# Performance work log

Measured on AMD Instinct MI355X. Metric: run time of the kernel, lower is better.

## Reference

```python
import jax, jax.numpy as jnp
import numpy as np

N, E, H, C, HC = 16384, 262144, 4, 128, 512
G, IN, ED, OUT, NCLS = 8, 5, 2, 256, 12
EPS = 1e-5


def _gatv2(x, src, dst, ea, Wl, Wr, We, att, b):
    # GATv2Conv (PyG): score = att . leaky_relu(lin_l(x_j) + lin_r(x_i) + lin_e(e))
    xl = (x @ Wl).reshape(-1, H, C)          # source transform [N,H,C]
    xr = (x @ Wr).reshape(-1, H, C)          # target transform [N,H,C]
    ee = (ea @ We).reshape(-1, H, C)         # edge embedding   [E,H,C]
    s = jax.nn.leaky_relu(xl[src] + xr[dst] + ee, 0.2)
    logit = jnp.einsum('ehc,hc->eh', s, att)            # [E,H]
    m = jax.ops.segment_max(logit, dst, num_segments=N)  # per-dst max
    a = jnp.exp(logit - m[dst])
    denom = jax.ops.segment_sum(a, dst, num_segments=N)
    alpha = a / (denom[dst] + 1e-16)                     # segment softmax
    out = jax.ops.segment_sum(xl[src] * alpha[:, :, None], dst, num_segments=N)
    return out.reshape(-1, HC) + b


def _bn(x, g, b):  # BatchNorm1d, training-mode batch stats
    mu = x.mean(0)
    var = x.var(0)
    return g * (x - mu) * jax.lax.rsqrt(var + EPS) + b


def setup_inputs() -> dict:
    key = jax.random.key(0)
    ks = iter(jax.random.split(key, 32))
    d = {}
    d['x'] = jax.random.normal(next(ks), (N, IN), jnp.float32)
    d['edge_attr'] = jax.random.normal(next(ks), (E, ED), jnp.float32)
    d['edge_index'] = jax.random.randint(next(ks), (2, E), 0, N)
    d['batch'] = jnp.sort(jax.random.randint(next(ks), (N,), 0, G))
    for i, din in zip((1, 2, 3), (IN, HC, HC)):
        d[f'c{i}_Wl'] = jax.random.normal(next(ks), (din, HC), jnp.float32) * 0.05
        d[f'c{i}_Wr'] = jax.random.normal(next(ks), (din, HC), jnp.float32) * 0.05
        d[f'c{i}_We'] = jax.random.normal(next(ks), (ED, HC), jnp.float32) * 0.05
        d[f'c{i}_att'] = jax.random.normal(next(ks), (H, C), jnp.float32) * 0.05
        d[f'c{i}_b'] = jnp.zeros((HC,), jnp.float32)
        d[f'bn{i}_g'] = jnp.ones((HC,), jnp.float32)
        d[f'bn{i}_b'] = jnp.zeros((HC,), jnp.float32)
    d['ge_W1'] = jax.random.normal(next(ks), (HC, OUT), jnp.float32) * 0.05
    d['ge_b1'] = jnp.zeros((OUT,), jnp.float32)
    d['ge_W2'] = jax.random.normal(next(ks), (OUT, OUT), jnp.float32) * 0.05
    d['ge_b2'] = jnp.zeros((OUT,), jnp.float32)
    d['cls_W'] = jax.random.normal(next(ks), (OUT, NCLS), jnp.float32) * 0.05
    d['cls_b'] = jnp.zeros((NCLS,), jnp.float32)
    return d


def reference(x, edge_attr, edge_index, batch,
              c1_Wl, c1_Wr, c1_We, c1_att, c1_b, bn1_g, bn1_b,
              c2_Wl, c2_Wr, c2_We, c2_att, c2_b, bn2_g, bn2_b,
              c3_Wl, c3_Wr, c3_We, c3_att, c3_b, bn3_g, bn3_b,
              ge_W1, ge_b1, ge_W2, ge_b2, cls_W, cls_b):
    src, dst = edge_index[0], edge_index[1]
    x1 = jax.nn.elu(_bn(_gatv2(x, src, dst, edge_attr, c1_Wl, c1_Wr, c1_We, c1_att, c1_b), bn1_g, bn1_b))
    x2 = jax.nn.elu(_bn(_gatv2(x1, src, dst, edge_attr, c2_Wl, c2_Wr, c2_We, c2_att, c2_b), bn2_g, bn2_b)) + x1
    x3 = jax.nn.elu(_bn(_gatv2(x2, src, dst, edge_attr, c3_Wl, c3_Wr, c3_We, c3_att, c3_b), bn3_g, bn3_b)) + x2
    cnt = jax.ops.segment_sum(jnp.ones((N,), x3.dtype), batch, num_segments=G)
    x_pool = jax.ops.segment_sum(x3, batch, num_segments=G) / cnt[:, None]
    emb = jax.nn.relu(x_pool @ ge_W1 + ge_b1) @ ge_W2 + ge_b2
    logits = emb @ cls_W + cls_b
    return logits, emb
```

## Files before the change

### kernel.cpp

```cpp
#include <hip/hip_runtime.h>
#include <math.h>

#define NN    16384
#define NE    262144
#define NHEAD 4
#define HC    512
#define NG    8

typedef __bf16 bf16x8 __attribute__((ext_vector_type(8)));
typedef float floatx4 __attribute__((ext_vector_type(4)));

__device__ __forceinline__ unsigned short f2bf(float f) {
    union { float f; unsigned u; } v{f};
    unsigned r = v.u + 0x7FFFu + ((v.u >> 16) & 1u);
    return (unsigned short)(r >> 16);
}

__device__ __forceinline__ void unpk8(uint4 v, float* f) {
    f[0] = __uint_as_float(v.x << 16); f[1] = __uint_as_float(v.x & 0xFFFF0000u);
    f[2] = __uint_as_float(v.y << 16); f[3] = __uint_as_float(v.y & 0xFFFF0000u);
    f[4] = __uint_as_float(v.z << 16); f[5] = __uint_as_float(v.z & 0xFFFF0000u);
    f[6] = __uint_as_float(v.w << 16); f[7] = __uint_as_float(v.w & 0xFFFF0000u);
}

__global__ void k_hist(const int* __restrict__ dst, int* __restrict__ cnt) {
    int e = blockIdx.x * 256 + threadIdx.x;
    if (e < NE) atomicAdd(&cnt[dst[e]], 1);
}

__global__ __launch_bounds__(1024) void k_scan(const int* __restrict__ cnt,
                                               int* __restrict__ rp,
                                               int* __restrict__ offp) {
    __shared__ int part[1024];
    int t = threadIdx.x;
    int base = t * 16;
    int loc[16];
    int s = 0;
#pragma unroll
    for (int i = 0; i < 16; i++) { loc[i] = s; s += cnt[base + i]; }
    part[t] = s;
    __syncthreads();
    for (int off = 1; off < 1024; off <<= 1) {
        int v = 0;
        if (t >= off) v = part[t - off];
        __syncthreads();
        if (t >= off) part[t] += v;
        __syncthreads();
    }
    int excl = (t == 0) ? 0 : part[t - 1];
#pragma unroll
    for (int i = 0; i < 16; i++) {
        int r = excl + loc[i];
        rp[base + i] = r;
        offp[base + i] = r;
    }
    if (t == 1023) rp[NN] = excl + s;
}

__global__ void k_fill(const int* __restrict__ dst, const int* __restrict__ src,
                       const float* __restrict__ ea, int* __restrict__ offp,
                       int* __restrict__ csrc, float2* __restrict__ ce) {
    int e = blockIdx.x * 256 + threadIdx.x;
    if (e < NE) {
        int d = dst[e];
        int pos = atomicAdd(&offp[d], 1);
        csrc[pos] = src[e];
        ce[pos] = *(const float2*)(ea + 2 * (size_t)e);
    }
}

__global__ void k_gcnt(const int* __restrict__ batch, int* __restrict__ gcnt) {
    int g = threadIdx.x;
    if (g < NG) {
        int lb[2];
#pragma unroll
        for (int q = 0; q < 2; q++) {
            int target = g + q;
            int lo = 0, hi = NN;
            while (lo < hi) {
                int mid = (lo + hi) >> 1;
                if (batch[mid] < target) lo = mid + 1; else hi = mid;
            }
            lb[q] = lo;
        }
        gcnt[g] = lb[1] - lb[0];
    }
}

__global__ __launch_bounds__(256) void k_lin1(const float* __restrict__ x,
                                              const float* __restrict__ Wl,
                                              const float* __restrict__ Wr,
                                              unsigned short* __restrict__ xl,
                                              unsigned short* __restrict__ xr) {
    int n = blockIdx.x;
    __shared__ float xs[8];
    if (threadIdx.x < 5) xs[threadIdx.x] = x[n * 5 + threadIdx.x];
    __syncthreads();
    for (int j = threadIdx.x; j < 512; j += 256) {
        float al = 0.f, ar = 0.f;
#pragma unroll
        for (int k = 0; k < 5; k++) {
            al += xs[k] * Wl[k * 512 + j];
            ar += xs[k] * Wr[k * 512 + j];
        }
        xl[(size_t)n * 512 + j] = f2bf(al);
        xr[(size_t)n * 512 + j] = f2bf(ar);
    }
}

__global__ __launch_bounds__(256) void k_wt(const float* __restrict__ W,
                                            unsigned short* __restrict__ Wt) {
    __shared__ float tile[64][65];
    int n0 = blockIdx.x * 64, k0 = blockIdx.y * 64;
    int lr = threadIdx.x >> 4;
    int lc = (threadIdx.x & 15) << 2;
    for (int r = lr; r < 64; r += 16) {
        float4 v = *(const float4*)(W + (size_t)(k0 + r) * 512 + n0 + lc);
        tile[r][lc] = v.x; tile[r][lc + 1] = v.y; tile[r][lc + 2] = v.z; tile[r][lc + 3] = v.w;
    }
    __syncthreads();
    for (int r = lr; r < 64; r += 16) {
        ushort4 o;
        o.x = f2bf(tile[lc + 0][r]); o.y = f2bf(tile[lc + 1][r]);
        o.z = f2bf(tile[lc + 2][r]); o.w = f2bf(tile[lc + 3][r]);
        *(ushort4*)(Wt + (size_t)(n0 + r) * 512 + k0 + lc) = o;
    }
}

#define BM 128
#define BN 128
#define BK 64
#define LDK 72

__global__ __launch_bounds__(256) void k_gemm_bf16(
        const unsigned short* __restrict__ Ab,
        const unsigned short* __restrict__ Bt,
        unsigned short* __restrict__ xl, unsigned short* __restrict__ xr) {
    __shared__ unsigned short As[BM * LDK];
    __shared__ unsigned short Bs[BN * LDK];
    int t = threadIdx.x;
    int bid = blockIdx.x;
    int xcd = bid & 7, r = bid >> 3;
    int m0 = (xcd * 16 + (r & 15)) * BM;
    int n0 = (r >> 4) * BN;
    int wid = t >> 6, lane = t & 63;
    int wm = (wid >> 1) * 64, wn = (wid & 1) * 64;
    int lrow = lane & 15, quad = lane >> 4;
    floatx4 acc[4][4] = {};
    for (int k0 = 0; k0 < 512; k0 += BK) {
        __syncthreads();
#pragma unroll
        for (int it = 0; it < 4; it++) {
            int cid = it * 256 + t;
            int row = cid >> 3, ch = cid & 7;
            uint4 va = *(const uint4*)(Ab + (size_t)(m0 + row) * 512 + k0 + ch * 8);
            *(uint4*)&As[row * LDK + ch * 8] = va;
            uint4 vb = *(const uint4*)(Bt + (size_t)(n0 + row) * 512 + k0 + ch * 8);
            *(uint4*)&Bs[row * LDK + ch * 8] = vb;
        }
        __syncthreads();
#pragma unroll
        for (int ko = 0; ko < 2; ko++) {
            bf16x8 af[4], bfr[4];
#pragma unroll
            for (int i = 0; i < 4; i++) {
                af[i]  = *(const bf16x8*)&As[(wm + i * 16 + lrow) * LDK + ko * 32 + quad * 8];
                bfr[i] = *(const bf16x8*)&Bs[(wn + i * 16 + lrow) * LDK + ko * 32 + quad * 8];
            }
#pragma unroll
            for (int i = 0; i < 4; i++)
#pragma unroll
                for (int j = 0; j < 4; j++)
                    acc[i][j] = __builtin_amdgcn_mfma_f32_16x16x32_bf16(af[i], bfr[j], acc[i][j], 0, 0, 0);
        }
    }
#pragma unroll
    for (int i = 0; i < 4; i++) {
        int row = m0 + wm + i * 16 + quad * 4;
#pragma unroll
        for (int j = 0; j < 4; j++) {
            int col = n0 + wn + j * 16 + lrow;
            unsigned short* dstp = (col < 512) ? (xl + (size_t)row * 512 + col)
                                               : (xr + (size_t)row * 512 + (col - 512));
#pragma unroll
            for (int rr = 0; rr < 4; rr++) dstp[(size_t)rr * 512] = f2bf(acc[i][j][rr]);
        }
    }
}

__global__ __launch_bounds__(256) void k_attn(
        const unsigned short* __restrict__ xl, const unsigned short* __restrict__ xr,
        const int* __restrict__ rp, const int* __restrict__ csrc,
        const float2* __restrict__ ce, const float* __restrict__ We,
        const float* __restrict__ att, const float* __restrict__ bias,
        float* __restrict__ out) {
    int n = blockIdx.x * 4 + (threadIdx.x >> 6);
    int lane = threadIdx.x & 63;
    int c0 = lane << 3;
    float wv0[8], wv1[8], av[8], rv[8];
    {
        float4 a = *(const float4*)(We + c0), b = *(const float4*)(We + c0 + 4);
        wv0[0]=a.x; wv0[1]=a.y; wv0[2]=a.z; wv0[3]=a.w; wv0[4]=b.x; wv0[5]=b.y; wv0[6]=b.z; wv0[7]=b.w;
        a = *(const float4*)(We + 512 + c0); b = *(const float4*)(We + 512 + c0 + 4);
        wv1[0]=a.x; wv1[1]=a.y; wv1[2]=a.z; wv1[3]=a.w; wv1[4]=b.x; wv1[5]=b.y; wv1[6]=b.z; wv1[7]=b.w;
        a = *(const float4*)(att + c0); b = *(const float4*)(att + c0 + 4);
        av[0]=a.x; av[1]=a.y; av[2]=a.z; av[3]=a.w; av[4]=b.x; av[5]=b.y; av[6]=b.z; av[7]=b.w;
        uint4 vr = *(const uint4*)(xr + (size_t)n * 512 + c0);
        unpk8(vr, rv);
    }
    float l = 0.f;
    float acc[8] = {0.f, 0.f, 0.f, 0.f, 0.f, 0.f, 0.f, 0.f};
    int beg = rp[n], end = rp[n + 1];
    uint4 cv0 = {}, cv1 = {};
    float2 ce0 = {}, ce1 = {};
    if (beg < end) {
        int i1 = (beg + 1 < end) ? beg + 1 : end - 1;
        cv0 = *(const uint4*)(xl + (size_t)csrc[beg] * 512 + c0);
        ce0 = ce[beg];
        cv1 = *(const uint4*)(xl + (size_t)csrc[i1] * 512 + c0);
        ce1 = ce[i1];
    }
    int i = beg;
    for (; i + 1 < end; i += 2) {
        uint4 a0 = cv0, a1 = cv1;
        float2 d0 = ce0, d1 = ce1;
        int q0 = i + 2, q1 = i + 3;
        q0 = (q0 < end) ? q0 : end - 1;
        q1 = (q1 < end) ? q1 : end - 1;
        cv0 = *(const uint4*)(xl + (size_t)csrc[q0] * 512 + c0);
        ce0 = ce[q0];
        cv1 = *(const uint4*)(xl + (size_t)csrc[q1] * 512 + c0);
        ce1 = ce[q1];
        float lv0[8], lv1[8];
        unpk8(a0, lv0);
        unpk8(a1, lv1);
        float p0 = 0.f, p1 = 0.f;
#pragma unroll
        for (int j = 0; j < 8; j++) {
            float v0 = lv0[j] + rv[j] + d0.x * wv0[j] + d0.y * wv1[j];
            float v1 = lv1[j] + rv[j] + d1.x * wv0[j] + d1.y * wv1[j];
            v0 = fmaxf(v0, 0.2f * v0);
            v1 = fmaxf(v1, 0.2f * v1);
            p0 += av[j] * v0;
            p1 += av[j] * v1;
        }
        p0 += __shfl_xor(p0, 1);  p1 += __shfl_xor(p1, 1);
        p0 += __shfl_xor(p0, 2);  p1 += __shfl_xor(p1, 2);
        p0 += __shfl_xor(p0, 4);  p1 += __shfl_xor(p1, 4);
        p0 += __shfl_xor(p0, 8);  p1 += __shfl_xor(p1, 8);
        float w0 = __expf(fminf(p0, 60.f));
        float w1 = __expf(fminf(p1, 60.f));
        l += w0 + w1;
#pragma unroll
        for (int j = 0; j < 8; j++)
            acc[j] += w0 * lv0[j] + w1 * lv1[j];
    }
    if (i < end) {
        float lv[8];
        unpk8(cv0, lv);
        float p = 0.f;
#pragma unroll
        for (int j = 0; j < 8; j++) {
            float v = lv[j] + rv[j] + ce0.x * wv0[j] + ce0.y * wv1[j];
            v = fmaxf(v, 0.2f * v);
            p += av[j] * v;
        }
        p += __shfl_xor(p, 1);
        p += __shfl_xor(p, 2);
        p += __shfl_xor(p, 4);
        p += __shfl_xor(p, 8);
        float w = __expf(fminf(p, 60.f));
        l += w;
#pragma unroll
        for (int j = 0; j < 8; j++) acc[j] += w * lv[j];
    }
    float inv = 1.f / (l + 1e-16f);
    const float* bb = bias + c0;
    float4 b0 = *(const float4*)bb, b1 = *(const float4*)(bb + 4);
    float* o = out + (size_t)n * 512 + c0;
    *(float4*)o = make_float4(acc[0] * inv + b0.x, acc[1] * inv + b0.y,
                              acc[2] * inv + b0.z, acc[3] * inv + b0.w);
    *(float4*)(o + 4) = make_float4(acc[4] * inv + b1.x, acc[5] * inv + b1.y,
                                    acc[6] * inv + b1.z, acc[7] * inv + b1.w);
}

__global__ __launch_bounds__(256) void k_bnstat(const float* __restrict__ x,
                                                double* __restrict__ sum,
                                                double* __restrict__ sumsq) {
    int t = threadIdx.x;
    int r0 = blockIdx.x * 64;
    float s0 = 0.f, s1 = 0.f, q0 = 0.f, q1 = 0.f;
    for (int r = r0; r < r0 + 64; r++) {
        float v0 = x[(size_t)r * 512 + t];
        float v1 = x[(size_t)r * 512 + t + 256];
        s0 += v0; q0 += v0 * v0;
        s1 += v1; q1 += v1 * v1;
    }
    atomicAdd(sum + t, (double)s0);
    atomicAdd(sum + t + 256, (double)s1);
    atomicAdd(sumsq + t, (double)q0);
    atomicAdd(sumsq + t + 256, (double)q1);
}

__global__ void k_bnfin(const double* __restrict__ sum, const double* __restrict__ sumsq,
                        const float* __restrict__ g, float* __restrict__ mean,
                        float* __restrict__ scale) {
    int c = blockIdx.x * 256 + threadIdx.x;
    if (c < 512) {
        double mu = sum[c] * (1.0 / NN);
        double var = sumsq[c] * (1.0 / NN) - mu * mu;
        mean[c] = (float)mu;
        scale[c] = g[c] * rsqrtf((float)var + 1e-5f);
    }
}

__global__ void k_bnapply(const float* __restrict__ v, const float* __restrict__ resid,
                          const float* __restrict__ mean, const float* __restrict__ scale,
                          const float* __restrict__ beta, float* __restrict__ out,
                          unsigned short* __restrict__ outb) {
    int i = (blockIdx.x * 256 + threadIdx.x) << 2;
    int c = i & 511;
    float4 vv = *(const float4*)(v + i);
    float4 mm = *(const float4*)(mean + c);
    float4 ss = *(const float4*)(scale + c);
    float4 be = *(const float4*)(beta + c);
    float y0 = (vv.x - mm.x) * ss.x + be.x;
    float y1 = (vv.y - mm.y) * ss.y + be.y;
    float y2 = (vv.z - mm.z) * ss.z + be.z;
    float y3 = (vv.w - mm.w) * ss.w + be.w;
    y0 = y0 > 0.f ? y0 : expm1f(y0);
    y1 = y1 > 0.f ? y1 : expm1f(y1);
    y2 = y2 > 0.f ? y2 : expm1f(y2);
    y3 = y3 > 0.f ? y3 : expm1f(y3);
    if (resid) {
        float4 rr = *(const float4*)(resid + i);
        y0 += rr.x; y1 += rr.y; y2 += rr.z; y3 += rr.w;
    }
    *(float4*)(out + i) = make_float4(y0, y1, y2, y3);
    if (outb) {
        ushort4 o;
        o.x = f2bf(y0); o.y = f2bf(y1); o.z = f2bf(y2); o.w = f2bf(y3);
        *(ushort4*)(outb + i) = o;
    }
}

__global__ __launch_bounds__(256) void k_pool(const float* __restrict__ x,
                                              const int* __restrict__ batch,
                                              float* __restrict__ pooled) {
    __shared__ float lacc[NG][512];
    int t = threadIdx.x;
    for (int i = t; i < NG * 512; i += 256) ((float*)lacc)[i] = 0.f;
    __syncthreads();
    int r0 = blockIdx.x * 64;
    for (int r = r0; r < r0 + 64; r++) {
        int g = batch[r];
        lacc[g][t] += x[(size_t)r * 512 + t];
        lacc[g][t + 256] += x[(size_t)r * 512 + t + 256];
    }
    __syncthreads();
    int gmin = batch[r0], gmax = batch[r0 + 63];
    for (int g = gmin; g <= gmax; g++)
        for (int i = t; i < 512; i += 256)
            atomicAdd(&pooled[g * 512 + i], lacc[g][i]);
}

__global__ __launch_bounds__(256) void k_mlp1(const float* __restrict__ pooled,
                                              const int* __restrict__ gcnt,
                                              const float* __restrict__ W1,
                                              const float* __restrict__ b1,
                                              float* __restrict__ h1) {
    int g = blockIdx.x, o = threadIdx.x;
    float dot = 0.f;
    for (int c = 0; c < 512; c++) dot += pooled[g * 512 + c] * W1[c * 256 + o];
    float s = dot / (float)gcnt[g] + b1[o];
    h1[g * 256 + o] = fmaxf(s, 0.f);
}

__global__ __launch_bounds__(256) void k_mlp2(const float* __restrict__ h1,
                                              const float* __restrict__ W2,
                                              const float* __restrict__ b2,
                                              float* __restrict__ emb) {
    int g = blockIdx.x, o = threadIdx.x;
    float s = b2[o];
    for (int c = 0; c < 256; c++) s += h1[g * 256 + c] * W2[c * 256 + o];
    emb[g * 256 + o] = s;
}

__global__ __launch_bounds__(128) void k_cls(const float* __restrict__ emb,
                                             const float* __restrict__ W,
                                             const float* __restrict__ b,
                                             float* __restrict__ out) {
    int t = threadIdx.x;
    if (t < NG * 12) {
        int g = t / 12, k = t % 12;
        float s = b[k];
        for (int c = 0; c < 256; c++) s += emb[g * 256 + c] * W[c * 12 + k];
        out[g * 12 + k] = s;
    }
}

extern "C" void kernel_launch(void* const* d_in, const int* in_sizes, int n_in,
                              void* d_out, int out_size, void* d_ws, size_t ws_size,
                              hipStream_t stream) {
    const float* x     = (const float*)d_in[0];
    const float* ea    = (const float*)d_in[1];
    const int*   ei    = (const int*)d_in[2];
    const int*   batch = (const int*)d_in[3];
    const int* src = ei;
    const int* dst = ei + NE;

    float* base = (float*)d_ws;
    size_t off = 0;
    auto alloc = [&](size_t n) -> float* {
        float* p = base + off;
        off += (n + 255) & ~(size_t)255;
        return p;
    };
    unsigned short* xl  = (unsigned short*)alloc((size_t)NN * 256);
    unsigned short* xr  = (unsigned short*)alloc((size_t)NN * 256);
    float*    bufA  = alloc((size_t)NN * 512);
    float*    bufB  = alloc((size_t)NN * 512);
    unsigned short* Xb  = (unsigned short*)alloc((size_t)NN * 256);
    unsigned short* Wt2 = (unsigned short*)alloc(512 * 1024 / 2);
    unsigned short* Wt3 = (unsigned short*)alloc(512 * 1024 / 2);
    int*      cnt   = (int*)alloc(NN);
    int*      rp    = (int*)alloc(NN + 1);
    int*      offp  = (int*)alloc(NN);
    int*      csrc  = (int*)alloc(NE);
    float2*   ce    = (float2*)alloc((size_t)NE * 2);
    double*   bsum  = (double*)alloc(1024);
    double*   bsq   = (double*)alloc(1024);
    float*    bmean = alloc(512);
    float*    bscale= alloc(512);
    float*    pooled= alloc(NG * 512);
    int*      gcnt  = (int*)alloc(NG);
    float*    h1    = alloc(NG * 256);
    float*    outp  = (float*)d_out;

    hipMemsetAsync(cnt, 0, NN * sizeof(int), stream);
    k_hist<<<NE / 256, 256, 0, stream>>>(dst, cnt);
    k_scan<<<1, 1024, 0, stream>>>(cnt, rp, offp);
    k_fill<<<NE / 256, 256, 0, stream>>>(dst, src, ea, offp, csrc, ce);
    k_gcnt<<<1, 64, 0, stream>>>(batch, gcnt);

    {
        dim3 wg(8, 8);
        k_wt<<<wg, 256, 0, stream>>>((const float*)d_in[11], Wt2);
        k_wt<<<wg, 256, 0, stream>>>((const float*)d_in[12], Wt2 + 512 * 512);
        k_wt<<<wg, 256, 0, stream>>>((const float*)d_in[18], Wt3);
        k_wt<<<wg, 256, 0, stream>>>((const float*)d_in[19], Wt3 + 512 * 512);
    }

    float* X = bufA;
    float* Y = bufB;
    for (int l = 0; l < 3; l++) {
        const float* Wl  = (const float*)d_in[4 + l * 7 + 0];
        const float* Wr  = (const float*)d_in[4 + l * 7 + 1];
        const float* We  = (const float*)d_in[4 + l * 7 + 2];
        const float* att = (const float*)d_in[4 + l * 7 + 3];
        const float* cb  = (const float*)d_in[4 + l * 7 + 4];
        const float* bg  = (const float*)d_in[4 + l * 7 + 5];
        const float* bb  = (const float*)d_in[4 + l * 7 + 6];

        if (l == 0) {
            k_lin1<<<NN, 256, 0, stream>>>(x, Wl, Wr, xl, xr);
        } else {
            k_gemm_bf16<<<1024, 256, 0, stream>>>(Xb, (l == 1) ? Wt2 : Wt3, xl, xr);
        }
        k_attn<<<NN / 4, 256, 0, stream>>>(xl, xr, rp, csrc, ce, We, att, cb, Y);

        hipMemsetAsync(bsum, 0, 1024 * sizeof(double), stream);
        k_bnstat<<<256, 256, 0, stream>>>(Y, bsum, bsq);
        k_bnfin<<<2, 256, 0, stream>>>(bsum, bsq, bg, bmean, bscale);
        k_bnapply<<<(size_t)NN * 512 / 1024, 256, 0, stream>>>(
            Y, (l == 0) ? nullptr : X, bmean, bscale, bb, Y,
            (l < 2) ? Xb : nullptr);

        float* tmp = X; X = Y; Y = tmp;
    }

    hipMemsetAsync(pooled, 0, NG * 512 * sizeof(float), stream);
    k_pool<<<NN / 64, 256, 0, stream>>>(X, batch, pooled);

    const float* geW1 = (const float*)d_in[25];
    const float* geb1 = (const float*)d_in[26];
    const float* geW2 = (const float*)d_in[27];
    const float* geb2 = (const float*)d_in[28];
    const float* clsW = (const float*)d_in[29];
    const float* clsb = (const float*)d_in[30];

    k_mlp1<<<NG, 256, 0, stream>>>(pooled, gcnt, geW1, geb1, h1);
    k_mlp2<<<NG, 256, 0, stream>>>(h1, geW2, geb2, outp + NG * 12);
    k_cls<<<1, 128, 0, stream>>>(outp + NG * 12, clsW, clsb, outp);
}
```

Baseline: 541.6 us.

## Fuse small kernels, use direct global-to-LDS loads with XOR swizzle in GEMM

Removes several tiny launches by merging k_gcnt into k_scan, the four transposes into one launch, bnfin into bnstat via a last-block counter, and mlp2 with cls into one head kernel. The per-layer memset is dropped because the last block zeroes the accumulators itself. k_lin1 is rewritten to have each wavefront compute one node with vectorised loads and stores. The GEMM now stages tiles with global_load_lds and an XOR-swizzled LDS layout in place of a padded register-staged copy. The trade-offs are extra atomics and a threadfence in bnstat, plus reliance on correct swizzle indexing.

```diff
diff --git a/kernel.cpp b/kernel.cpp
--- a/kernel.cpp
+++ b/kernel.cpp
@@ -23,6 +23,12 @@
     f[6] = __uint_as_float(v.w << 16); f[7] = __uint_as_float(v.w & 0xFFFF0000u);
 }
 
+__device__ __forceinline__ void gl_lds16(const unsigned short* g, unsigned short* l) {
+    __builtin_amdgcn_global_load_lds(
+        (const __attribute__((address_space(1))) unsigned int*)g,
+        (__attribute__((address_space(3))) unsigned int*)l, 16, 0, 0);
+}
+
 __global__ void k_hist(const int* __restrict__ dst, int* __restrict__ cnt) {
     int e = blockIdx.x * 256 + threadIdx.x;
     if (e < NE) atomicAdd(&cnt[dst[e]], 1);
@@ -30,9 +36,25 @@
 
 __global__ __launch_bounds__(1024) void k_scan(const int* __restrict__ cnt,
                                                int* __restrict__ rp,
-                                               int* __restrict__ offp) {
+                                               int* __restrict__ offp,
+                                               const int* __restrict__ batch,
+                                               int* __restrict__ gcnt) {
     __shared__ int part[1024];
     int t = threadIdx.x;
+    if (t < NG) {
+        int lb[2];
+#pragma unroll
+        for (int q = 0; q < 2; q++) {
+            int target = t + q;
+            int lo = 0, hi = NN;
+            while (lo < hi) {
+                int mid = (lo + hi) >> 1;
+                if (batch[mid] < target) lo = mid + 1; else hi = mid;
+            }
+            lb[q] = lo;
+        }
+        gcnt[t] = lb[1] - lb[0];
+    }
     int base = t * 16;
     int loc[16];
     int s = 0;
@@ -69,49 +91,53 @@
     }
 }
 
-__global__ void k_gcnt(const int* __restrict__ batch, int* __restrict__ gcnt) {
-    int g = threadIdx.x;
-    if (g < NG) {
-        int lb[2];
-#pragma unroll
-        for (int q = 0; q < 2; q++) {
-            int target = g + q;
-            int lo = 0, hi = NN;
-            while (lo < hi) {
-                int mid = (lo + hi) >> 1;
-                if (batch[mid] < target) lo = mid + 1; else hi = mid;
-            }
-            lb[q] = lo;
-        }
-        gcnt[g] = lb[1] - lb[0];
-    }
-}
-
 __global__ __launch_bounds__(256) void k_lin1(const float* __restrict__ x,
                                               const float* __restrict__ Wl,
                                               const float* __restrict__ Wr,
                                               unsigned short* __restrict__ xl,
                                               unsigned short* __restrict__ xr) {
-    int n = blockIdx.x;
-    __shared__ float xs[8];
-    if (threadIdx.x < 5) xs[threadIdx.x] = x[n * 5 + threadIdx.x];
-    __syncthreads();
-    for (int j = threadIdx.x; j < 512; j += 256) {
-        float al = 0.f, ar = 0.f;
-#pragma unroll
-        for (int k = 0; k < 5; k++) {
-            al += xs[k] * Wl[k * 512 + j];
-            ar += xs[k] * Wr[k * 512 + j];
-        }
-        xl[(size_t)n * 512 + j] = f2bf(al);
-        xr[(size_t)n * 512 + j] = f2bf(ar);
-    }
-}
-
-__global__ __launch_bounds__(256) void k_wt(const float* __restrict__ W,
-                                            unsigned short* __restrict__ Wt) {
+    int n = blockIdx.x * 4 + (threadIdx.x >> 6);
+    int lane = threadIdx.x & 63;
+    int j0 = lane << 3;
+    float xs[5];
+#pragma unroll
+    for (int k = 0; k < 5; k++) xs[k] = x[n * 5 + k];
+    float al[8] = {}, ar[8] = {};
+#pragma unroll
+    for (int k = 0; k < 5; k++) {
+        float4 wl0 = *(const float4*)(Wl + k * 512 + j0);
+        float4 wl1 = *(const float4*)(Wl + k * 512 + j0 + 4);
+        float4 wr0 = *(const float4*)(Wr + k * 512 + j0);
+        float4 wr1 = *(const float4*)(Wr + k * 512 + j0 + 4);
+        al[0] += xs[k] * wl0.x; al[1] += xs[k] * wl0.y; al[2] += xs[k] * wl0.z; al[3] += xs[k] * wl0.w;
+        al[4] += xs[k] * wl1.x; al[5] += xs[k] * wl1.y; al[6] += xs[k] * wl1.z; al[7] += xs[k] * wl1.w;
+        ar[0] += xs[k] * wr0.x; ar[1] += xs[k] * wr0.y; ar[2] += xs[k] * wr0.z; ar[3] += xs[k] * wr0.w;
+        ar[4] += xs[k] * wr1.x; ar[5] += xs[k] * wr1.y; ar[6] += xs[k] * wr1.z; ar[7] += xs[k] * wr1.w;
+    }
+    ushort4 o0, o1;
+    o0.x = f2bf(al[0]); o0.y = f2bf(al[1]); o0.z = f2bf(al[2]); o0.w = f2bf(al[3]);
+    o1.x = f2bf(al[4]); o1.y = f2bf(al[5]); o1.z = f2bf(al[6]); o1.w = f2bf(al[7]);
+    *(ushort4*)(xl + (size_t)n * 512 + j0) = o0;
+    *(ushort4*)(xl + (size_t)n * 512 + j0 + 4) = o1;
+    o0.x = f2bf(ar[0]); o0.y = f2bf(ar[1]); o0.z = f2bf(ar[2]); o0.w = f2bf(ar[3]);
+    o1.x = f2bf(ar[4]); o1.y = f2bf(ar[5]); o1.z = f2bf(ar[6]); o1.w = f2bf(ar[7]);
+    *(ushort4*)(xr + (size_t)n * 512 + j0) = o0;
+    *(ushort4*)(xr + (size_t)n * 512 + j0 + 4) = o1;
+}
+
+__global__ __launch_bounds__(256) void k_wt4(const float* __restrict__ W0,
+                                             const float* __restrict__ W1,
+                                             const float* __restrict__ W2,
+                                             const float* __restrict__ W3,
+                                             unsigned short* __restrict__ Wt2,
+                                             unsigned short* __restrict__ Wt3) {
     __shared__ float tile[64][65];
-    int n0 = blockIdx.x * 64, k0 = blockIdx.y * 64;
+    int bid = blockIdx.x;
+    int mat = bid >> 6, sub = bid & 63;
+    const float* W = (mat == 0) ? W0 : (mat == 1) ? W1 : (mat == 2) ? W2 : W3;
+    unsigned short* Wt = (mat == 0) ? Wt2 : (mat == 1) ? (Wt2 + 512 * 512)
+                       : (mat == 2) ? Wt3 : (Wt3 + 512 * 512);
+    int n0 = (sub & 7) * 64, k0 = (sub >> 3) * 64;
     int lr = threadIdx.x >> 4;
     int lc = (threadIdx.x & 15) << 2;
     for (int r = lr; r < 64; r += 16) {
@@ -129,43 +155,43 @@
 
 #define BM 128
 #define BN 128
-#define BK 64
-#define LDK 72
 
 __global__ __launch_bounds__(256) void k_gemm_bf16(
         const unsigned short* __restrict__ Ab,
         const unsigned short* __restrict__ Bt,
         unsigned short* __restrict__ xl, unsigned short* __restrict__ xr) {
-    __shared__ unsigned short As[BM * LDK];
-    __shared__ unsigned short Bs[BN * LDK];
+    __shared__ unsigned short As[BM * 64];
+    __shared__ unsigned short Bs[BN * 64];
     int t = threadIdx.x;
     int bid = blockIdx.x;
-    int xcd = bid & 7, r = bid >> 3;
-    int m0 = (xcd * 16 + (r & 15)) * BM;
-    int n0 = (r >> 4) * BN;
-    int wid = t >> 6, lane = t & 63;
-    int wm = (wid >> 1) * 64, wn = (wid & 1) * 64;
+    int xcd = bid & 7, rr_ = bid >> 3;
+    int m0 = (xcd * 16 + (rr_ & 15)) * BM;
+    int n0 = (rr_ >> 4) * BN;
+    int wv = t >> 6, lane = t & 63;
+    int wm = (wv >> 1) * 64, wn = (wv & 1) * 64;
     int lrow = lane & 15, quad = lane >> 4;
+    int lr = lane >> 3;
+    int lc = lane & 7;
+    int cg = lc ^ lr;
     floatx4 acc[4][4] = {};
-    for (int k0 = 0; k0 < 512; k0 += BK) {
+    for (int k0 = 0; k0 < 512; k0 += 64) {
         __syncthreads();
 #pragma unroll
         for (int it = 0; it < 4; it++) {
-            int cid = it * 256 + t;
-            int row = cid >> 3, ch = cid & 7;
-            uint4 va = *(const uint4*)(Ab + (size_t)(m0 + row) * 512 + k0 + ch * 8);
-            *(uint4*)&As[row * LDK + ch * 8] = va;
-            uint4 vb = *(const uint4*)(Bt + (size_t)(n0 + row) * 512 + k0 + ch * 8);
-            *(uint4*)&Bs[row * LDK + ch * 8] = vb;
+            int rb = wv * 4 + it;
+            int row = rb * 8 + lr;
+            gl_lds16(Ab + (size_t)(m0 + row) * 512 + k0 + cg * 8, As + rb * 512);
+            gl_lds16(Bt + (size_t)(n0 + row) * 512 + k0 + cg * 8, Bs + rb * 512);
         }
         __syncthreads();
 #pragma unroll
         for (int ko = 0; ko < 2; ko++) {
             bf16x8 af[4], bfr[4];
+            int cp = ((ko * 4 + quad) ^ (lrow & 7)) * 8;
 #pragma unroll
             for (int i = 0; i < 4; i++) {
-                af[i]  = *(const bf16x8*)&As[(wm + i * 16 + lrow) * LDK + ko * 32 + quad * 8];
-                bfr[i] = *(const bf16x8*)&Bs[(wn + i * 16 + lrow) * LDK + ko * 32 + quad * 8];
+                af[i]  = *(const bf16x8*)&As[(wm + i * 16 + lrow) * 64 + cp];
+                bfr[i] = *(const bf16x8*)&Bs[(wn + i * 16 + lrow) * 64 + cp];
             }
 #pragma unroll
             for (int i = 0; i < 4; i++)
@@ -183,7 +209,7 @@
             unsigned short* dstp = (col < 512) ? (xl + (size_t)row * 512 + col)
                                                : (xr + (size_t)row * 512 + (col - 512));
 #pragma unroll
-            for (int rr = 0; rr < 4; rr++) dstp[(size_t)rr * 512] = f2bf(acc[i][j][rr]);
+            for (int r = 0; r < 4; r++) dstp[(size_t)r * 512] = f2bf(acc[i][j][r]);
         }
     }
 }
@@ -286,7 +312,11 @@
 
 __global__ __launch_bounds__(256) void k_bnstat(const float* __restrict__ x,
                                                 double* __restrict__ sum,
-                                                double* __restrict__ sumsq) {
+                                                double* __restrict__ sumsq,
+                                                int* __restrict__ counter,
+                                                const float* __restrict__ g,
+                                                float* __restrict__ mean,
+                                                float* __restrict__ scale) {
     int t = threadIdx.x;
     int r0 = blockIdx.x * 64;
     float s0 = 0.f, s1 = 0.f, q0 = 0.f, q1 = 0.f;
@@ -300,17 +330,21 @@
     atomicAdd(sum + t + 256, (double)s1);
     atomicAdd(sumsq + t, (double)q0);
     atomicAdd(sumsq + t + 256, (double)q1);
-}
-
-__global__ void k_bnfin(const double* __restrict__ sum, const double* __restrict__ sumsq,
-                        const float* __restrict__ g, float* __restrict__ mean,
-                        float* __restrict__ scale) {
-    int c = blockIdx.x * 256 + threadIdx.x;
-    if (c < 512) {
-        double mu = sum[c] * (1.0 / NN);
-        double var = sumsq[c] * (1.0 / NN) - mu * mu;
-        mean[c] = (float)mu;
-        scale[c] = g[c] * rsqrtf((float)var + 1e-5f);
+    __threadfence();
+    __syncthreads();
+    __shared__ int isLast;
+    if (t == 0) isLast = (atomicAdd(counter, 1) == 255);
+    __syncthreads();
+    if (isLast) {
+        for (int c = t; c < 512; c += 256) {
+            double s = __longlong_as_double(atomicExch((unsigned long long*)(sum + c), 0ull));
+            double q = __longlong_as_double(atomicExch((unsigned long long*)(sumsq + c), 0ull));
+            double mu = s * (1.0 / NN);
+            double var = q * (1.0 / NN) - mu * mu;
+            mean[c] = (float)mu;
+            scale[c] = g[c] * rsqrtf((float)var + 1e-5f);
+        }
+        if (t == 0) atomicExch(counter, 0);
     }
 }
 
@@ -376,26 +410,23 @@
     h1[g * 256 + o] = fmaxf(s, 0.f);
 }
 
-__global__ __launch_bounds__(256) void k_mlp2(const float* __restrict__ h1,
+__global__ __launch_bounds__(256) void k_head(const float* __restrict__ h1,
                                               const float* __restrict__ W2,
                                               const float* __restrict__ b2,
-                                              float* __restrict__ emb) {
+                                              const float* __restrict__ clsW,
+                                              const float* __restrict__ clsb,
+                                              float* __restrict__ outp) {
+    __shared__ float es[256];
     int g = blockIdx.x, o = threadIdx.x;
     float s = b2[o];
     for (int c = 0; c < 256; c++) s += h1[g * 256 + c] * W2[c * 256 + o];
-    emb[g * 256 + o] = s;
-}
-
-__global__ __launch_bounds__(128) void k_cls(const float* __restrict__ emb,
-                                             const float* __restrict__ W,
-                                             const float* __restrict__ b,
-                                             float* __restrict__ out) {
-    int t = threadIdx.x;
-    if (t < NG * 12) {
-        int g = t / 12, k = t % 12;
-        float s = b[k];
-        for (int c = 0; c < 256; c++) s += emb[g * 256 + c] * W[c * 12 + k];
-        out[g * 12 + k] = s;
+    outp[NG * 12 + g * 256 + o] = s;
+    es[o] = s;
+    __syncthreads();
+    if (o < 12) {
+        float lg = clsb[o];
+        for (int c = 0; c < 256; c++) lg += es[c] * clsW[c * 12 + o];
+        outp[g * 12 + o] = lg;
     }
 }
 
@@ -428,8 +459,9 @@
     int*      offp  = (int*)alloc(NN);
     int*      csrc  = (int*)alloc(NE);
     float2*   ce    = (float2*)alloc((size_t)NE * 2);
-    double*   bsum  = (double*)alloc(1024);
-    double*   bsq   = (double*)alloc(1024);
+    double*   bsum  = (double*)alloc(2048);
+    double*   bsq   = bsum + 512;
+    int*      bcnt  = (int*)alloc(64);
     float*    bmean = alloc(512);
     float*    bscale= alloc(512);
     float*    pooled= alloc(NG * 512);
@@ -438,18 +470,12 @@
     float*    outp  = (float*)d_out;
 
     hipMemsetAsync(cnt, 0, NN * sizeof(int), stream);
+    hipMemsetAsync(bsum, 0, 2048 * sizeof(float) + 64 * sizeof(int), stream);
     k_hist<<<NE / 256, 256, 0, stream>>>(dst, cnt);
-    k_scan<<<1, 1024, 0, stream>>>(cnt, rp, offp);
+    k_scan<<<1, 1024, 0, stream>>>(cnt, rp, offp, batch, gcnt);
     k_fill<<<NE / 256, 256, 0, stream>>>(dst, src, ea, offp, csrc, ce);
-    k_gcnt<<<1, 64, 0, stream>>>(batch, gcnt);
-
-    {
-        dim3 wg(8, 8);
-        k_wt<<<wg, 256, 0, stream>>>((const float*)d_in[11], Wt2);
-        k_wt<<<wg, 256, 0, stream>>>((const float*)d_in[12], Wt2 + 512 * 512);
-        k_wt<<<wg, 256, 0, stream>>>((const float*)d_in[18], Wt3);
-        k_wt<<<wg, 256, 0, stream>>>((const float*)d_in[19], Wt3 + 512 * 512);
-    }
+    k_wt4<<<256, 256, 0, stream>>>((const float*)d_in[11], (const float*)d_in[12],
+                                   (const float*)d_in[18], (const float*)d_in[19], Wt2, Wt3);
 
     float* X = bufA;
     float* Y = bufB;
@@ -463,15 +489,13 @@
         const float* bb  = (const float*)d_in[4 + l * 7 + 6];
 
         if (l == 0) {
-            k_lin1<<<NN, 256, 0, stream>>>(x, Wl, Wr, xl, xr);
+            k_lin1<<<NN / 4, 256, 0, stream>>>(x, Wl, Wr, xl, xr);
         } else {
             k_gemm_bf16<<<1024, 256, 0, stream>>>(Xb, (l == 1) ? Wt2 : Wt3, xl, xr);
         }
         k_attn<<<NN / 4, 256, 0, stream>>>(xl, xr, rp, csrc, ce, We, att, cb, Y);
 
-        hipMemsetAsync(bsum, 0, 1024 * sizeof(double), stream);
-        k_bnstat<<<256, 256, 0, stream>>>(Y, bsum, bsq);
-        k_bnfin<<<2, 256, 0, stream>>>(bsum, bsq, bg, bmean, bscale);
+        k_bnstat<<<256, 256, 0, stream>>>(Y, bsum, bsq, bcnt, bg, bmean, bscale);
         k_bnapply<<<(size_t)NN * 512 / 1024, 256, 0, stream>>>(
             Y, (l == 0) ? nullptr : X, bmean, bscale, bb, Y,
             (l < 2) ? Xb : nullptr);
@@ -490,6 +514,5 @@
     const float* clsb = (const float*)d_in[30];
 
     k_mlp1<<<NG, 256, 0, stream>>>(pooled, gcnt, geW1, geb1, h1);
-    k_mlp2<<<NG, 256, 0, stream>>>(h1, geW2, geb2, outp + NG * 12);
-    k_cls<<<1, 128, 0, stream>>>(outp + NG * 12, clsW, clsb, outp);
-}
+    k_head<<<NG, 256, 0, stream>>>(h1, geW2, geb2, clsW, clsb, outp);
+}
```

After: 578.2 us. 1.07x slower.
